# Optimization experiments

Hardware: AMD Instinct MI355X
Metric: run time of the kernel (lower is better)

## Reference

```python
import jax, jax.numpy as jnp
import numpy as np

N_NODES = 50000
N_EDGES = 800000
N_FEAT = 128
HIDDEN = 64
N_CLASSES = 16


def setup_inputs() -> dict:
    key = jax.random.key(0)
    ks = jax.random.split(key, 8)
    x = jax.random.normal(ks[0], (N_NODES, N_FEAT), dtype=jnp.float32)
    edge_index = jax.random.randint(ks[1], (2, N_EDGES), 0, N_NODES, dtype=jnp.int64)
    # GCNConv weights (glorot-like) and biases
    W1 = jax.random.normal(ks[2], (N_FEAT, HIDDEN), dtype=jnp.float32) / np.sqrt(N_FEAT)
    b1 = jnp.zeros((HIDDEN,), dtype=jnp.float32)
    W2 = jax.random.normal(ks[3], (HIDDEN, HIDDEN), dtype=jnp.float32) / np.sqrt(HIDDEN)
    b2 = jnp.zeros((HIDDEN,), dtype=jnp.float32)
    Wout = jax.random.normal(ks[4], (HIDDEN, N_CLASSES), dtype=jnp.float32) / np.sqrt(HIDDEN)
    bout = jnp.zeros((N_CLASSES,), dtype=jnp.float32)
    return {"x": x, "edge_index": edge_index, "W1": W1, "b1": b1,
            "W2": W2, "b2": b2, "Wout": Wout, "bout": bout}


def _gcn_conv(h, src, dst, norm, W, b, n_nodes):
    # h: [N, F_in]; linear transform then normalized scatter-add aggregation
    h = h @ W                                   # [N, F_out]
    msg = h[src] * norm[:, None]                # gather + scale  [E+N, F_out]
    out = jax.ops.segment_sum(msg, dst, num_segments=n_nodes)  # scatter-add
    return out + b


def reference(x, edge_index, W1, b1, W2, b2, Wout, bout):
    n = x.shape[0]
    # add self-loops (PyG GCNConv default add_self_loops=True)
    loops = jnp.arange(n, dtype=edge_index.dtype)
    src = jnp.concatenate([edge_index[0], loops])
    dst = jnp.concatenate([edge_index[1], loops])
    # symmetric normalization: deg^-1/2[src] * deg^-1/2[dst] (edge_weight = 1)
    ones = jnp.ones(src.shape[0], dtype=x.dtype)
    deg = jax.ops.segment_sum(ones, dst, num_segments=n)
    dinv = jnp.where(deg > 0, jax.lax.rsqrt(jnp.maximum(deg, 1e-12)), 0.0)
    norm = dinv[src] * dinv[dst]

    h = _gcn_conv(x, src, dst, norm, W1, b1, n)
    h = jax.nn.relu(h)
    # dropout p=0.5 with training=False -> identity
    h = _gcn_conv(h, src, dst, norm, W2, b2, n)
    h = jax.nn.relu(h)
    logits = h @ Wout + bout
    return jax.nn.softmax(logits, axis=1)
```

## Files before the change

kernel.cpp:

```cpp
#include <hip/hip_runtime.h>
#include <hip/hip_fp16.h>

#define N_NODES 50000
#define N_EDGES 800000
#define N_FEAT 128
#define HIDDEN 64
#define N_CLASSES 16
#define NBLK_NODE 196
#define TCAP 8192

typedef _Float16 f16x8 __attribute__((ext_vector_type(8)));
typedef float f32x4 __attribute__((ext_vector_type(4)));

__global__ void k_init(int* __restrict__ tileCur) {
    int tid = threadIdx.x;
    if (tid < NBLK_NODE) tileCur[tid] = tid * TCAP;
}

__global__ __launch_bounds__(256) void k_part(const int* __restrict__ ei,
                                              int* __restrict__ tileCur,
                                              int* __restrict__ binned) {
    __shared__ int cnt[NBLK_NODE], base[NBLK_NODE], cur[NBLK_NODE];
    int tid = threadIdx.x;
    int start = blockIdx.x * 4096;
    if (tid < NBLK_NODE) cnt[tid] = 0;
    __syncthreads();
    int s[16], d[16];
#pragma unroll
    for (int u = 0; u < 4; ++u) {
        int e0 = start + u * 1024 + tid * 4;
        if (e0 + 4 <= N_EDGES) {
            int4 s4 = *(const int4*)&ei[e0];
            int4 d4 = *(const int4*)&ei[N_EDGES + e0];
            s[u * 4 + 0] = s4.x; s[u * 4 + 1] = s4.y; s[u * 4 + 2] = s4.z; s[u * 4 + 3] = s4.w;
            d[u * 4 + 0] = d4.x; d[u * 4 + 1] = d4.y; d[u * 4 + 2] = d4.z; d[u * 4 + 3] = d4.w;
#pragma unroll
            for (int q = 0; q < 4; ++q) atomicAdd(&cnt[d[u * 4 + q] >> 8], 1);
        } else {
#pragma unroll
            for (int q = 0; q < 4; ++q) {
                int e = e0 + q;
                if (e < N_EDGES) {
                    s[u * 4 + q] = ei[e];
                    d[u * 4 + q] = ei[N_EDGES + e];
                    atomicAdd(&cnt[d[u * 4 + q] >> 8], 1);
                } else s[u * 4 + q] = -1;
            }
        }
    }
    __syncthreads();
    if (tid < NBLK_NODE) {
        base[tid] = atomicAdd(&tileCur[tid], cnt[tid]);
        cur[tid] = 0;
    }
    __syncthreads();
#pragma unroll
    for (int u = 0; u < 16; ++u) {
        if (s[u] < 0) continue;
        int t = d[u] >> 8;
        int r = atomicAdd(&cur[t], 1);
        int p = base[t] + r;
        if (p < (t + 1) * TCAP)
            binned[p] = s[u] | ((d[u] & 255) << 16);
    }
}

__global__ __launch_bounds__(256) void k_finesort(const int* __restrict__ binned,
                                                  const int* __restrict__ tileCur,
                                                  int* __restrict__ csr,
                                                  int2* __restrict__ rse,
                                                  float* __restrict__ dinv) {
    __shared__ int stage[TCAP];
    __shared__ int sc[256];
    __shared__ int cnt256[256];
    __shared__ int nodeOff[256];
    int tid = threadIdx.x;
    int tb = blockIdx.x;
    int beg = tb * TCAP;
    int m = tileCur[tb] - beg;
    if (m > TCAP) m = TCAP;
    cnt256[tid] = 0;
    __syncthreads();
    const int4* b4 = (const int4*)(binned + beg);
    int nv = m >> 2;
    for (int i = tid; i < nv; i += 256) {
        int4 r = b4[i];
        atomicAdd(&cnt256[(r.x >> 16) & 255], 1);
        atomicAdd(&cnt256[(r.y >> 16) & 255], 1);
        atomicAdd(&cnt256[(r.z >> 16) & 255], 1);
        atomicAdd(&cnt256[(r.w >> 16) & 255], 1);
    }
    for (int i = (m & ~3) + tid; i < m; i += 256)
        atomicAdd(&cnt256[(binned[beg + i] >> 16) & 255], 1);
    __syncthreads();
    int myc = cnt256[tid];
    sc[tid] = myc;
    __syncthreads();
#pragma unroll
    for (int off = 1; off < 256; off <<= 1) {
        int t = (tid >= off) ? sc[tid - off] : 0;
        __syncthreads();
        sc[tid] += t;
        __syncthreads();
    }
    int off0 = sc[tid] - myc;
    nodeOff[tid] = off0;
    int gnode = tb * 256 + tid;
    if (gnode < N_NODES) {
        dinv[gnode] = rsqrtf((float)myc + 1.0f);
        rse[gnode] = make_int2(beg + off0, myc);
    }
    cnt256[tid] = 0;
    __syncthreads();
    for (int i = tid; i < nv; i += 256) {
        int4 r = b4[i];
        int rr;
        rr = atomicAdd(&cnt256[(r.x >> 16) & 255], 1); stage[nodeOff[(r.x >> 16) & 255] + rr] = r.x & 0xFFFF;
        rr = atomicAdd(&cnt256[(r.y >> 16) & 255], 1); stage[nodeOff[(r.y >> 16) & 255] + rr] = r.y & 0xFFFF;
        rr = atomicAdd(&cnt256[(r.z >> 16) & 255], 1); stage[nodeOff[(r.z >> 16) & 255] + rr] = r.z & 0xFFFF;
        rr = atomicAdd(&cnt256[(r.w >> 16) & 255], 1); stage[nodeOff[(r.w >> 16) & 255] + rr] = r.w & 0xFFFF;
    }
    for (int i = (m & ~3) + tid; i < m; i += 256) {
        int rec = binned[beg + i];
        int dl = (rec >> 16) & 255;
        int rr = atomicAdd(&cnt256[dl], 1);
        stage[nodeOff[dl] + rr] = rec & 0xFFFF;
    }
    __syncthreads();
    int4* c4 = (int4*)(csr + beg);
    for (int i = tid; i < nv; i += 256) c4[i] = ((const int4*)stage)[i];
    for (int i = (m & ~3) + tid; i < m; i += 256) csr[beg + i] = stage[i];
}

template <int K, typename TIn>
__global__ __launch_bounds__(256) void k_mm(const TIn* __restrict__ a,
                                            const float* __restrict__ w,
                                            const float* __restrict__ dinv,
                                            __half* __restrict__ out) {
    constexpr int LDK = K + 8;
    __shared__ __align__(16) __half A_lds[64 * LDK];
    __shared__ __align__(16) __half Wt_lds[64 * LDK];
    int tid = threadIdx.x;
    long nbase = (long)blockIdx.x * 64;

    for (int i = tid; i < K * 16; i += 256) {
        int k = (i * 4) >> 6;
        int f0 = (i * 4) & 63;
        float4 v = *(const float4*)&w[i * 4];
        Wt_lds[(f0 + 0) * LDK + k] = __float2half(v.x);
        Wt_lds[(f0 + 1) * LDK + k] = __float2half(v.y);
        Wt_lds[(f0 + 2) * LDK + k] = __float2half(v.z);
        Wt_lds[(f0 + 3) * LDK + k] = __float2half(v.w);
    }
    for (int i = tid; i < 64 * K / 8; i += 256) {
        int n = (i * 8) / K;
        int k0 = (i * 8) % K;
        long gn = nbase + n;
        if constexpr (sizeof(TIn) == 4) {
            float4 v0, v1;
            if (gn < N_NODES) {
                v0 = *(const float4*)&a[gn * K + k0];
                v1 = *(const float4*)&a[gn * K + k0 + 4];
            } else {
                v0 = make_float4(0.f, 0.f, 0.f, 0.f);
                v1 = v0;
            }
            __half2* dst = (__half2*)&A_lds[n * LDK + k0];
            dst[0] = __floats2half2_rn(v0.x, v0.y);
            dst[1] = __floats2half2_rn(v0.z, v0.w);
            dst[2] = __floats2half2_rn(v1.x, v1.y);
            dst[3] = __floats2half2_rn(v1.z, v1.w);
        } else {
            int4 v = (gn < N_NODES) ? *(const int4*)&a[gn * K + k0]
                                    : make_int4(0, 0, 0, 0);
            *(int4*)&A_lds[n * LDK + k0] = v;
        }
    }
    __syncthreads();

    int wv = tid >> 6;
    int lane = tid & 63;
    int m = lane & 15;
    int quad = lane >> 4;
    const __half* Arow = &A_lds[(wv * 16 + m) * LDK + quad * 8];
    f32x4 acc[4] = {};
#pragma unroll
    for (int t = 0; t < K; t += 32) {
        f16x8 af = *(const f16x8*)(const void*)&Arow[t];
#pragma unroll
        for (int g = 0; g < 4; ++g) {
            f16x8 bf = *(const f16x8*)(const void*)&Wt_lds[(g * 16 + m) * LDK + t + quad * 8];
            acc[g] = __builtin_amdgcn_mfma_f32_16x16x32_f16(af, bf, acc[g], 0, 0, 0);
        }
    }

#pragma unroll
    for (int r = 0; r < 4; ++r) {
        int n = wv * 16 + quad * 4 + r;
        long gn = nbase + n;
        if (gn < N_NODES) {
            float di = dinv[gn];
#pragma unroll
            for (int g = 0; g < 4; ++g)
                out[gn * HIDDEN + g * 16 + m] = __float2half(acc[g][r] * di);
        }
    }
}

__device__ __forceinline__ void acc_row8(float* a, int4 rv) {
    float2 f;
    f = __half22float2(*(__half2*)&rv.x); a[0] += f.x; a[1] += f.y;
    f = __half22float2(*(__half2*)&rv.y); a[2] += f.x; a[3] += f.y;
    f = __half22float2(*(__half2*)&rv.z); a[4] += f.x; a[5] += f.y;
    f = __half22float2(*(__half2*)&rv.w); a[6] += f.x; a[7] += f.y;
}

__global__ void k_gather(const __half* __restrict__ h, const int* __restrict__ csr,
                         const int2* __restrict__ rse, const float* __restrict__ dinv,
                         const float* __restrict__ bias, __half* __restrict__ out) {
    int t = blockIdx.x * 256 + threadIdx.x;
    int node = __builtin_amdgcn_readfirstlane(t >> 6);
    int lane = t & 63;
    int e8 = lane >> 3;
    int q = lane & 7;
    int2 se = rse[node];
    int r0 = se.x, r1 = se.x + se.y;
    float dd = dinv[node];

    float a[8] = {0.f, 0.f, 0.f, 0.f, 0.f, 0.f, 0.f, 0.f};
    if (e8 == 0)
        acc_row8(a, *(const int4*)&h[(long)node * HIDDEN + q * 8]);

    int j = r0;
    while (j + 16 <= r1) {
        int sA = csr[j + e8];
        int sB = csr[j + 8 + e8];
        int4 rA = *(const int4*)&h[(long)sA * HIDDEN + q * 8];
        int4 rB = *(const int4*)&h[(long)sB * HIDDEN + q * 8];
        acc_row8(a, rA);
        acc_row8(a, rB);
        j += 16;
    }
    if (j + 8 <= r1) {
        int sA = csr[j + e8];
        acc_row8(a, *(const int4*)&h[(long)sA * HIDDEN + q * 8]);
        j += 8;
    }
    int rem = r1 - j;
    if (e8 < rem) {
        int sA = csr[j + e8];
        acc_row8(a, *(const int4*)&h[(long)sA * HIDDEN + q * 8]);
    }
#pragma unroll
    for (int off = 8; off < 64; off <<= 1)
#pragma unroll
        for (int i = 0; i < 8; ++i) a[i] += __shfl_xor(a[i], off, 64);

    if (e8 == 0) {
        float4 b0 = *(const float4*)&bias[q * 8];
        float4 b1 = *(const float4*)&bias[q * 8 + 4];
        float r[8];
        r[0] = fmaxf(fmaf(a[0], dd, b0.x), 0.f);
        r[1] = fmaxf(fmaf(a[1], dd, b0.y), 0.f);
        r[2] = fmaxf(fmaf(a[2], dd, b0.z), 0.f);
        r[3] = fmaxf(fmaf(a[3], dd, b0.w), 0.f);
        r[4] = fmaxf(fmaf(a[4], dd, b1.x), 0.f);
        r[5] = fmaxf(fmaf(a[5], dd, b1.y), 0.f);
        r[6] = fmaxf(fmaf(a[6], dd, b1.z), 0.f);
        r[7] = fmaxf(fmaf(a[7], dd, b1.w), 0.f);
        __half2 h0 = __floats2half2_rn(r[0], r[1]);
        __half2 h1 = __floats2half2_rn(r[2], r[3]);
        __half2 h2 = __floats2half2_rn(r[4], r[5]);
        __half2 h3 = __floats2half2_rn(r[6], r[7]);
        int4 o;
        o.x = *(int*)&h0; o.y = *(int*)&h1; o.z = *(int*)&h2; o.w = *(int*)&h3;
        *(int4*)&out[(long)node * HIDDEN + q * 8] = o;
    }
}

__global__ void k_out(const __half* __restrict__ h, const float* __restrict__ w,
                      const float* __restrict__ b, float* __restrict__ out) {
    __shared__ float Ws[HIDDEN * N_CLASSES];
    __shared__ float bs[N_CLASSES];
    int tid = threadIdx.x;
    for (int i = tid; i < HIDDEN * N_CLASSES; i += 256) Ws[i] = w[i];
    if (tid < N_CLASSES) bs[tid] = b[tid];
    __syncthreads();
    int node = blockIdx.x * 16 + (tid >> 4);
    int c = tid & 15;
    const __half* hr = h + (long)node * HIDDEN;
    float acc = bs[c];
#pragma unroll
    for (int k = 0; k < HIDDEN; ++k)
        acc = fmaf(__half2float(hr[k]), Ws[k * N_CLASSES + c], acc);
    float m = acc;
#pragma unroll
    for (int off = 8; off; off >>= 1) m = fmaxf(m, __shfl_xor(m, off, 16));
    float ex = expf(acc - m);
    float s = ex;
#pragma unroll
    for (int off = 8; off; off >>= 1) s += __shfl_xor(s, off, 16);
    out[(long)node * N_CLASSES + c] = ex / s;
}

extern "C" void kernel_launch(void* const* d_in, const int* in_sizes, int n_in,
                              void* d_out, int out_size, void* d_ws, size_t ws_size,
                              hipStream_t stream) {
    const float* x    = (const float*)d_in[0];
    const int*   ei   = (const int*)d_in[1];
    const float* W1   = (const float*)d_in[2];
    const float* b1   = (const float*)d_in[3];
    const float* W2   = (const float*)d_in[4];
    const float* b2   = (const float*)d_in[5];
    const float* Wout = (const float*)d_in[6];
    const float* bout = (const float*)d_in[7];
    float* out = (float*)d_out;

    char* ws = (char*)d_ws;
    int2*   rse     = (int2*)ws;                       ws += 400128;
    float*  dinv    = (float*)ws;                      ws += 200192;
    int*    tileCur = (int*)ws;                        ws += 1024;
    int*    csr     = (int*)ws;                        ws += (size_t)NBLK_NODE * TCAP * 4;
    char*   slotA   = ws;                              ws += 6553600;
    __half* bufB    = (__half*)ws;
    int*    binned  = (int*)slotA;
    __half* bufA    = (__half*)slotA;

    const int NB_MM = (N_NODES + 63) / 64;
    const int NB_E16 = (N_EDGES + 4095) / 4096;

    k_init<<<1, 256, 0, stream>>>(tileCur);
    k_part<<<NB_E16, 256, 0, stream>>>(ei, tileCur, binned);
    k_finesort<<<NBLK_NODE, 256, 0, stream>>>(binned, tileCur, csr, rse, dinv);

    k_mm<N_FEAT, float><<<NB_MM, 256, 0, stream>>>(x, W1, dinv, bufA);
    k_gather<<<N_NODES / 4, 256, 0, stream>>>(bufA, csr, rse, dinv, b1, bufB);

    k_mm<HIDDEN, __half><<<NB_MM, 256, 0, stream>>>(bufB, W2, dinv, bufA);
    k_gather<<<N_NODES / 4, 256, 0, stream>>>(bufA, csr, rse, dinv, b2, bufB);

    k_out<<<N_NODES / 16, 256, 0, stream>>>(bufB, Wout, bout, out);
}
```

Baseline: 170.5 us.

## Fuse second aggregation with output projection and softmax; single-pass finesort with 512 threads

The second gather kernel now also computes the output linear layer and the softmax in registers. This removes the separate k_out launch and the write and re-read of the hidden fp16 buffer. Separately, the fine sort runs with 512 threads and keeps each record and its atomic rank in registers, so the bin is read from global memory once instead of twice. It also replaces the shared-memory block scan with a wave shuffle scan. The cost is higher register pressure in both kernels, and the fixed 4x512 int4 register loop assumes each tile holds at most TCAP entries.

```diff
diff --git a/kernel.cpp b/kernel.cpp
--- a/kernel.cpp
+++ b/kernel.cpp
@@ -65,71 +65,87 @@
     }
 }
 
-__global__ __launch_bounds__(256) void k_finesort(const int* __restrict__ binned,
+__global__ __launch_bounds__(512) void k_finesort(const int* __restrict__ binned,
                                                   const int* __restrict__ tileCur,
                                                   int* __restrict__ csr,
                                                   int2* __restrict__ rse,
                                                   float* __restrict__ dinv) {
     __shared__ int stage[TCAP];
-    __shared__ int sc[256];
     __shared__ int cnt256[256];
     __shared__ int nodeOff[256];
+    __shared__ int wsum[4];
     int tid = threadIdx.x;
     int tb = blockIdx.x;
     int beg = tb * TCAP;
     int m = tileCur[tb] - beg;
     if (m > TCAP) m = TCAP;
-    cnt256[tid] = 0;
+    if (tid < 256) cnt256[tid] = 0;
     __syncthreads();
     const int4* b4 = (const int4*)(binned + beg);
     int nv = m >> 2;
-    for (int i = tid; i < nv; i += 256) {
-        int4 r = b4[i];
-        atomicAdd(&cnt256[(r.x >> 16) & 255], 1);
-        atomicAdd(&cnt256[(r.y >> 16) & 255], 1);
-        atomicAdd(&cnt256[(r.z >> 16) & 255], 1);
-        atomicAdd(&cnt256[(r.w >> 16) & 255], 1);
-    }
-    for (int i = (m & ~3) + tid; i < m; i += 256)
-        atomicAdd(&cnt256[(binned[beg + i] >> 16) & 255], 1);
-    __syncthreads();
-    int myc = cnt256[tid];
-    sc[tid] = myc;
-    __syncthreads();
-#pragma unroll
-    for (int off = 1; off < 256; off <<= 1) {
-        int t = (tid >= off) ? sc[tid - off] : 0;
-        __syncthreads();
-        sc[tid] += t;
-        __syncthreads();
-    }
-    int off0 = sc[tid] - myc;
-    nodeOff[tid] = off0;
-    int gnode = tb * 256 + tid;
-    if (gnode < N_NODES) {
-        dinv[gnode] = rsqrtf((float)myc + 1.0f);
-        rse[gnode] = make_int2(beg + off0, myc);
-    }
-    cnt256[tid] = 0;
-    __syncthreads();
-    for (int i = tid; i < nv; i += 256) {
-        int4 r = b4[i];
-        int rr;
-        rr = atomicAdd(&cnt256[(r.x >> 16) & 255], 1); stage[nodeOff[(r.x >> 16) & 255] + rr] = r.x & 0xFFFF;
-        rr = atomicAdd(&cnt256[(r.y >> 16) & 255], 1); stage[nodeOff[(r.y >> 16) & 255] + rr] = r.y & 0xFFFF;
-        rr = atomicAdd(&cnt256[(r.z >> 16) & 255], 1); stage[nodeOff[(r.z >> 16) & 255] + rr] = r.z & 0xFFFF;
-        rr = atomicAdd(&cnt256[(r.w >> 16) & 255], 1); stage[nodeOff[(r.w >> 16) & 255] + rr] = r.w & 0xFFFF;
-    }
-    for (int i = (m & ~3) + tid; i < m; i += 256) {
-        int rec = binned[beg + i];
-        int dl = (rec >> 16) & 255;
-        int rr = atomicAdd(&cnt256[dl], 1);
-        stage[nodeOff[dl] + rr] = rec & 0xFFFF;
-    }
+    int4 v[4], rk[4];
+#pragma unroll
+    for (int u = 0; u < 4; ++u) {
+        int i = tid + u * 512;
+        if (i < nv) {
+            int4 r = b4[i];
+            v[u] = r;
+            rk[u].x = atomicAdd(&cnt256[(r.x >> 16) & 255], 1);
+            rk[u].y = atomicAdd(&cnt256[(r.y >> 16) & 255], 1);
+            rk[u].z = atomicAdd(&cnt256[(r.z >> 16) & 255], 1);
+            rk[u].w = atomicAdd(&cnt256[(r.w >> 16) & 255], 1);
+        }
+    }
+    int tailrec = -1, tailrk = 0;
+    int ti = (m & ~3) + tid;
+    if (ti < m) {
+        tailrec = binned[beg + ti];
+        tailrk = atomicAdd(&cnt256[(tailrec >> 16) & 255], 1);
+    }
+    __syncthreads();
+    int myc = 0, sc = 0;
+    if (tid < 256) {
+        myc = cnt256[tid];
+        sc = myc;
+#pragma unroll
+        for (int off = 1; off < 64; off <<= 1) {
+            int tv = __shfl_up(sc, off, 64);
+            if ((tid & 63) >= off) sc += tv;
+        }
+        if ((tid & 63) == 63) wsum[tid >> 6] = sc;
+    }
+    __syncthreads();
+    if (tid < 256) {
+        int wv = tid >> 6;
+        int pre = 0;
+        if (wv > 0) pre += wsum[0];
+        if (wv > 1) pre += wsum[1];
+        if (wv > 2) pre += wsum[2];
+        int off0 = sc - myc + pre;
+        nodeOff[tid] = off0;
+        int gnode = tb * 256 + tid;
+        if (gnode < N_NODES) {
+            dinv[gnode] = rsqrtf((float)myc + 1.0f);
+            rse[gnode] = make_int2(beg + off0, myc);
+        }
+    }
+    __syncthreads();
+#pragma unroll
+    for (int u = 0; u < 4; ++u) {
+        int i = tid + u * 512;
+        if (i < nv) {
+            stage[nodeOff[(v[u].x >> 16) & 255] + rk[u].x] = v[u].x & 0xFFFF;
+            stage[nodeOff[(v[u].y >> 16) & 255] + rk[u].y] = v[u].y & 0xFFFF;
+            stage[nodeOff[(v[u].z >> 16) & 255] + rk[u].z] = v[u].z & 0xFFFF;
+            stage[nodeOff[(v[u].w >> 16) & 255] + rk[u].w] = v[u].w & 0xFFFF;
+        }
+    }
+    if (tailrec >= 0)
+        stage[nodeOff[(tailrec >> 16) & 255] + tailrk] = tailrec & 0xFFFF;
     __syncthreads();
     int4* c4 = (int4*)(csr + beg);
-    for (int i = tid; i < nv; i += 256) c4[i] = ((const int4*)stage)[i];
-    for (int i = (m & ~3) + tid; i < m; i += 256) csr[beg + i] = stage[i];
+    for (int i = tid; i < nv; i += 512) c4[i] = ((const int4*)stage)[i];
+    for (int i = (m & ~3) + tid; i < m; i += 512) csr[beg + i] = stage[i];
 }
 
 template <int K, typename TIn>
@@ -278,29 +294,90 @@
     }
 }
 
-__global__ void k_out(const __half* __restrict__ h, const float* __restrict__ w,
-                      const float* __restrict__ b, float* __restrict__ out) {
-    __shared__ float Ws[HIDDEN * N_CLASSES];
-    __shared__ float bs[N_CLASSES];
-    int tid = threadIdx.x;
-    for (int i = tid; i < HIDDEN * N_CLASSES; i += 256) Ws[i] = w[i];
-    if (tid < N_CLASSES) bs[tid] = b[tid];
-    __syncthreads();
-    int node = blockIdx.x * 16 + (tid >> 4);
-    int c = tid & 15;
-    const __half* hr = h + (long)node * HIDDEN;
-    float acc = bs[c];
-#pragma unroll
-    for (int k = 0; k < HIDDEN; ++k)
-        acc = fmaf(__half2float(hr[k]), Ws[k * N_CLASSES + c], acc);
-    float m = acc;
-#pragma unroll
-    for (int off = 8; off; off >>= 1) m = fmaxf(m, __shfl_xor(m, off, 16));
-    float ex = expf(acc - m);
-    float s = ex;
-#pragma unroll
-    for (int off = 8; off; off >>= 1) s += __shfl_xor(s, off, 16);
-    out[(long)node * N_CLASSES + c] = ex / s;
+__global__ void k_gather_out(const __half* __restrict__ h, const int* __restrict__ csr,
+                             const int2* __restrict__ rse, const float* __restrict__ dinv,
+                             const float* __restrict__ bias,
+                             const float* __restrict__ wout, const float* __restrict__ bout,
+                             float* __restrict__ out) {
+    int t = blockIdx.x * 256 + threadIdx.x;
+    int node = __builtin_amdgcn_readfirstlane(t >> 6);
+    int lane = t & 63;
+    int e8 = lane >> 3;
+    int q = lane & 7;
+    int c0 = e8 * 2;
+    float2 wcol[8];
+#pragma unroll
+    for (int i = 0; i < 8; ++i)
+        wcol[i] = *(const float2*)&wout[(q * 8 + i) * N_CLASSES + c0];
+    float2 bb = *(const float2*)&bout[c0];
+
+    int2 se = rse[node];
+    int r0 = se.x, r1 = se.x + se.y;
+    float dd = dinv[node];
+
+    float a[8] = {0.f, 0.f, 0.f, 0.f, 0.f, 0.f, 0.f, 0.f};
+    if (e8 == 0)
+        acc_row8(a, *(const int4*)&h[(long)node * HIDDEN + q * 8]);
+
+    int j = r0;
+    while (j + 16 <= r1) {
+        int sA = csr[j + e8];
+        int sB = csr[j + 8 + e8];
+        int4 rA = *(const int4*)&h[(long)sA * HIDDEN + q * 8];
+        int4 rB = *(const int4*)&h[(long)sB * HIDDEN + q * 8];
+        acc_row8(a, rA);
+        acc_row8(a, rB);
+        j += 16;
+    }
+    if (j + 8 <= r1) {
+        int sA = csr[j + e8];
+        acc_row8(a, *(const int4*)&h[(long)sA * HIDDEN + q * 8]);
+        j += 8;
+    }
+    int rem = r1 - j;
+    if (e8 < rem) {
+        int sA = csr[j + e8];
+        acc_row8(a, *(const int4*)&h[(long)sA * HIDDEN + q * 8]);
+    }
+#pragma unroll
+    for (int off = 8; off < 64; off <<= 1)
+#pragma unroll
+        for (int i = 0; i < 8; ++i) a[i] += __shfl_xor(a[i], off, 64);
+
+    float4 b0 = *(const float4*)&bias[q * 8];
+    float4 b1 = *(const float4*)&bias[q * 8 + 4];
+    float r[8];
+    r[0] = fmaxf(fmaf(a[0], dd, b0.x), 0.f);
+    r[1] = fmaxf(fmaf(a[1], dd, b0.y), 0.f);
+    r[2] = fmaxf(fmaf(a[2], dd, b0.z), 0.f);
+    r[3] = fmaxf(fmaf(a[3], dd, b0.w), 0.f);
+    r[4] = fmaxf(fmaf(a[4], dd, b1.x), 0.f);
+    r[5] = fmaxf(fmaf(a[5], dd, b1.y), 0.f);
+    r[6] = fmaxf(fmaf(a[6], dd, b1.z), 0.f);
+    r[7] = fmaxf(fmaf(a[7], dd, b1.w), 0.f);
+
+    float l0 = 0.f, l1 = 0.f;
+#pragma unroll
+    for (int i = 0; i < 8; ++i) {
+        l0 = fmaf(r[i], wcol[i].x, l0);
+        l1 = fmaf(r[i], wcol[i].y, l1);
+    }
+#pragma unroll
+    for (int off = 1; off < 8; off <<= 1) {
+        l0 += __shfl_xor(l0, off, 64);
+        l1 += __shfl_xor(l1, off, 64);
+    }
+    l0 += bb.x;
+    l1 += bb.y;
+    float mx = fmaxf(l0, l1);
+#pragma unroll
+    for (int off = 8; off < 64; off <<= 1) mx = fmaxf(mx, __shfl_xor(mx, off, 64));
+    float e0 = expf(l0 - mx), e1 = expf(l1 - mx);
+    float s = e0 + e1;
+#pragma unroll
+    for (int off = 8; off < 64; off <<= 1) s += __shfl_xor(s, off, 64);
+    if (q == 0)
+        *(float2*)&out[(long)node * N_CLASSES + c0] = make_float2(e0 / s, e1 / s);
 }
 
 extern "C" void kernel_launch(void* const* d_in, const int* in_sizes, int n_in,
@@ -331,13 +408,11 @@
 
     k_init<<<1, 256, 0, stream>>>(tileCur);
     k_part<<<NB_E16, 256, 0, stream>>>(ei, tileCur, binned);
-    k_finesort<<<NBLK_NODE, 256, 0, stream>>>(binned, tileCur, csr, rse, dinv);
+    k_finesort<<<NBLK_NODE, 512, 0, stream>>>(binned, tileCur, csr, rse, dinv);
 
     k_mm<N_FEAT, float><<<NB_MM, 256, 0, stream>>>(x, W1, dinv, bufA);
     k_gather<<<N_NODES / 4, 256, 0, stream>>>(bufA, csr, rse, dinv, b1, bufB);
 
     k_mm<HIDDEN, __half><<<NB_MM, 256, 0, stream>>>(bufB, W2, dinv, bufA);
-    k_gather<<<N_NODES / 4, 256, 0, stream>>>(bufA, csr, rse, dinv, b2, bufB);
-
-    k_out<<<N_NODES / 16, 256, 0, stream>>>(bufB, Wout, bout, out);
-}
+    k_gather_out<<<N_NODES / 4, 256, 0, stream>>>(bufA, csr, rse, dinv, b2, Wout, bout, out);
+}
```

Measured after the change: 200.9 us. 17.9% more time.

## Split hidden features into two 32-wide planes for cache-friendly gather

Applied to the files above, without the earlier changes.

Stores the hidden activations as two feature-planes of 32 halves per node instead of one 64-wide row, and splits each gather into two blocks, one per plane. Consecutive blocks (interleaved via blockIdx bits) handle the same plane, so each gather pass touches a working set half the size, meant to improve L2/MALL hit rates for the random neighbour reads. The cost is twice as many gather blocks, each reading the CSR index lists and rse again, and narrower 8-byte loads per lane.

```diff
diff --git a/kernel.cpp b/kernel.cpp
--- a/kernel.cpp
+++ b/kernel.cpp
@@ -8,6 +8,7 @@
 #define N_CLASSES 16
 #define NBLK_NODE 196
 #define TCAP 8192
+#define PLANE (N_NODES * 32)
 
 typedef _Float16 f16x8 __attribute__((ext_vector_type(8)));
 typedef float f32x4 __attribute__((ext_vector_type(4)));
@@ -171,7 +172,8 @@
             dst[2] = __floats2half2_rn(v1.x, v1.y);
             dst[3] = __floats2half2_rn(v1.z, v1.w);
         } else {
-            int4 v = (gn < N_NODES) ? *(const int4*)&a[gn * K + k0]
+            const __half* ap = (const __half*)a + (long)(k0 >> 5) * PLANE;
+            int4 v = (gn < N_NODES) ? *(const int4*)&ap[gn * 32 + (k0 & 31)]
                                     : make_int4(0, 0, 0, 0);
             *(int4*)&A_lds[n * LDK + k0] = v;
         }
@@ -202,79 +204,75 @@
             float di = dinv[gn];
 #pragma unroll
             for (int g = 0; g < 4; ++g)
-                out[gn * HIDDEN + g * 16 + m] = __float2half(acc[g][r] * di);
+                out[(long)(g >> 1) * PLANE + gn * 32 + (g & 1) * 16 + m] =
+                    __float2half(acc[g][r] * di);
         }
     }
 }
 
-__device__ __forceinline__ void acc_row8(float* a, int4 rv) {
+__device__ __forceinline__ void acc_row4(float* a, int2 rv) {
     float2 f;
     f = __half22float2(*(__half2*)&rv.x); a[0] += f.x; a[1] += f.y;
     f = __half22float2(*(__half2*)&rv.y); a[2] += f.x; a[3] += f.y;
-    f = __half22float2(*(__half2*)&rv.z); a[4] += f.x; a[5] += f.y;
-    f = __half22float2(*(__half2*)&rv.w); a[6] += f.x; a[7] += f.y;
 }
 
 __global__ void k_gather(const __half* __restrict__ h, const int* __restrict__ csr,
                          const int2* __restrict__ rse, const float* __restrict__ dinv,
                          const float* __restrict__ bias, __half* __restrict__ out) {
-    int t = blockIdx.x * 256 + threadIdx.x;
-    int node = __builtin_amdgcn_readfirstlane(t >> 6);
+    int b = blockIdx.x;
+    int x = b & 7;
+    int half = x >> 2;
+    int nb = (b >> 3) * 4 + (x & 3);
+    int t = threadIdx.x;
+    int node = __builtin_amdgcn_readfirstlane(nb * 4 + (t >> 6));
     int lane = t & 63;
     int e8 = lane >> 3;
     int q = lane & 7;
+    const __half* hp = h + (long)half * PLANE;
     int2 se = rse[node];
     int r0 = se.x, r1 = se.x + se.y;
     float dd = dinv[node];
 
-    float a[8] = {0.f, 0.f, 0.f, 0.f, 0.f, 0.f, 0.f, 0.f};
+    float a[4] = {0.f, 0.f, 0.f, 0.f};
     if (e8 == 0)
-        acc_row8(a, *(const int4*)&h[(long)node * HIDDEN + q * 8]);
+        acc_row4(a, *(const int2*)&hp[(long)node * 32 + q * 4]);
 
     int j = r0;
     while (j + 16 <= r1) {
         int sA = csr[j + e8];
         int sB = csr[j + 8 + e8];
-        int4 rA = *(const int4*)&h[(long)sA * HIDDEN + q * 8];
-        int4 rB = *(const int4*)&h[(long)sB * HIDDEN + q * 8];
-        acc_row8(a, rA);
-        acc_row8(a, rB);
+        int2 rA = *(const int2*)&hp[(long)sA * 32 + q * 4];
+        int2 rB = *(const int2*)&hp[(long)sB * 32 + q * 4];
+        acc_row4(a, rA);
+        acc_row4(a, rB);
         j += 16;
     }
     if (j + 8 <= r1) {
         int sA = csr[j + e8];
-        acc_row8(a, *(const int4*)&h[(long)sA * HIDDEN + q * 8]);
+        acc_row4(a, *(const int2*)&hp[(long)sA * 32 + q * 4]);
         j += 8;
     }
     int rem = r1 - j;
     if (e8 < rem) {
         int sA = csr[j + e8];
-        acc_row8(a, *(const int4*)&h[(long)sA * HIDDEN + q * 8]);
+        acc_row4(a, *(const int2*)&hp[(long)sA * 32 + q * 4]);
     }
 #pragma unroll
     for (int off = 8; off < 64; off <<= 1)
 #pragma unroll
-        for (int i = 0; i < 8; ++i) a[i] += __shfl_xor(a[i], off, 64);
+        for (int i = 0; i < 4; ++i) a[i] += __shfl_xor(a[i], off, 64);
 
     if (e8 == 0) {
-        float4 b0 = *(const float4*)&bias[q * 8];
-        float4 b1 = *(const float4*)&bias[q * 8 + 4];
-        float r[8];
-        r[0] = fmaxf(fmaf(a[0], dd, b0.x), 0.f);
-        r[1] = fmaxf(fmaf(a[1], dd, b0.y), 0.f);
-        r[2] = fmaxf(fmaf(a[2], dd, b0.z), 0.f);
-        r[3] = fmaxf(fmaf(a[3], dd, b0.w), 0.f);
-        r[4] = fmaxf(fmaf(a[4], dd, b1.x), 0.f);
-        r[5] = fmaxf(fmaf(a[5], dd, b1.y), 0.f);
-        r[6] = fmaxf(fmaf(a[6], dd, b1.z), 0.f);
-        r[7] = fmaxf(fmaf(a[7], dd, b1.w), 0.f);
-        __half2 h0 = __floats2half2_rn(r[0], r[1]);
-        __half2 h1 = __floats2half2_rn(r[2], r[3]);
-        __half2 h2 = __floats2half2_rn(r[4], r[5]);
-        __half2 h3 = __floats2half2_rn(r[6], r[7]);
-        int4 o;
-        o.x = *(int*)&h0; o.y = *(int*)&h1; o.z = *(int*)&h2; o.w = *(int*)&h3;
-        *(int4*)&out[(long)node * HIDDEN + q * 8] = o;
+        float4 bv = *(const float4*)&bias[half * 32 + q * 4];
+        float r0f = fmaxf(fmaf(a[0], dd, bv.x), 0.f);
+        float r1f = fmaxf(fmaf(a[1], dd, bv.y), 0.f);
+        float r2f = fmaxf(fmaf(a[2], dd, bv.z), 0.f);
+        float r3f = fmaxf(fmaf(a[3], dd, bv.w), 0.f);
+        __half2 h0 = __floats2half2_rn(r0f, r1f);
+        __half2 h1 = __floats2half2_rn(r2f, r3f);
+        int2 o;
+        o.x = *(int*)&h0; o.y = *(int*)&h1;
+        *(int2*)&out[(long)half * PLANE + (long)node * 32 + q * 4] = o;
     }
 }
 
@@ -288,11 +286,15 @@
     __syncthreads();
     int node = blockIdx.x * 16 + (tid >> 4);
     int c = tid & 15;
-    const __half* hr = h + (long)node * HIDDEN;
+    const __half* hr0 = h + (long)node * 32;
+    const __half* hr1 = h + (long)PLANE + (long)node * 32;
     float acc = bs[c];
 #pragma unroll
-    for (int k = 0; k < HIDDEN; ++k)
-        acc = fmaf(__half2float(hr[k]), Ws[k * N_CLASSES + c], acc);
+    for (int k = 0; k < 32; ++k)
+        acc = fmaf(__half2float(hr0[k]), Ws[k * N_CLASSES + c], acc);
+#pragma unroll
+    for (int k = 0; k < 32; ++k)
+        acc = fmaf(__half2float(hr1[k]), Ws[(k + 32) * N_CLASSES + c], acc);
     float m = acc;
 #pragma unroll
     for (int off = 8; off; off >>= 1) m = fmaxf(m, __shfl_xor(m, off, 16));
@@ -328,16 +330,17 @@
 
     const int NB_MM = (N_NODES + 63) / 64;
     const int NB_E16 = (N_EDGES + 4095) / 4096;
+    const int NB_GATHER = 2 * (N_NODES / 4);
 
     k_init<<<1, 256, 0, stream>>>(tileCur);
     k_part<<<NB_E16, 256, 0, stream>>>(ei, tileCur, binned);
     k_finesort<<<NBLK_NODE, 256, 0, stream>>>(binned, tileCur, csr, rse, dinv);
 
     k_mm<N_FEAT, float><<<NB_MM, 256, 0, stream>>>(x, W1, dinv, bufA);
-    k_gather<<<N_NODES / 4, 256, 0, stream>>>(bufA, csr, rse, dinv, b1, bufB);
+    k_gather<<<NB_GATHER, 256, 0, stream>>>(bufA, csr, rse, dinv, b1, bufB);
 
     k_mm<HIDDEN, __half><<<NB_MM, 256, 0, stream>>>(bufB, W2, dinv, bufA);
-    k_gather<<<N_NODES / 4, 256, 0, stream>>>(bufA, csr, rse, dinv, b2, bufB);
+    k_gather<<<NB_GATHER, 256, 0, stream>>>(bufA, csr, rse, dinv, b2, bufB);
 
     k_out<<<N_NODES / 16, 256, 0, stream>>>(bufB, Wout, bout, out);
 }
```

Result: slower. 191.4 us (+12.3%).

## Fuse finesort with first matmul and move source dinv scaling into gather

Applied to the files above, without the earlier changes.

Merges the CSR fine-sort kernel and the first feature matmul into one launch with shared dynamic LDS. Blocks below NBLK_NODE sort and the rest compute x@W1, so the two independent stages overlap. To remove the matmul's dependence on dinv, the source-side degree scaling moves into the gather, which now loads dinv[src] per edge and uses FMA. binned now gets its own workspace region instead of aliasing bufA. The cost is an extra scattered dinv load per edge in both gathers.

```diff
diff --git a/kernel.cpp b/kernel.cpp
--- a/kernel.cpp
+++ b/kernel.cpp
@@ -65,17 +65,16 @@
     }
 }
 
-__global__ __launch_bounds__(256) void k_finesort(const int* __restrict__ binned,
-                                                  const int* __restrict__ tileCur,
-                                                  int* __restrict__ csr,
-                                                  int2* __restrict__ rse,
-                                                  float* __restrict__ dinv) {
-    __shared__ int stage[TCAP];
-    __shared__ int sc[256];
-    __shared__ int cnt256[256];
-    __shared__ int nodeOff[256];
-    int tid = threadIdx.x;
-    int tb = blockIdx.x;
+__device__ __forceinline__ void finesort_body(int tb, const int* __restrict__ binned,
+                                              const int* __restrict__ tileCur,
+                                              int* __restrict__ csr,
+                                              int2* __restrict__ rse,
+                                              float* __restrict__ dinv, char* smem) {
+    int* stage   = (int*)smem;
+    int* sc      = stage + TCAP;
+    int* cnt256  = sc + 256;
+    int* nodeOff = cnt256 + 256;
+    int tid = threadIdx.x;
     int beg = tb * TCAP;
     int m = tileCur[tb] - beg;
     if (m > TCAP) m = TCAP;
@@ -133,15 +132,14 @@
 }
 
 template <int K, typename TIn>
-__global__ __launch_bounds__(256) void k_mm(const TIn* __restrict__ a,
-                                            const float* __restrict__ w,
-                                            const float* __restrict__ dinv,
-                                            __half* __restrict__ out) {
+__device__ __forceinline__ void mm_body(int bx, const TIn* __restrict__ a,
+                                        const float* __restrict__ w,
+                                        __half* __restrict__ out, char* smem) {
     constexpr int LDK = K + 8;
-    __shared__ __align__(16) __half A_lds[64 * LDK];
-    __shared__ __align__(16) __half Wt_lds[64 * LDK];
-    int tid = threadIdx.x;
-    long nbase = (long)blockIdx.x * 64;
+    __half* A_lds  = (__half*)smem;
+    __half* Wt_lds = A_lds + 64 * LDK;
+    int tid = threadIdx.x;
+    long nbase = (long)bx * 64;
 
     for (int i = tid; i < K * 16; i += 256) {
         int k = (i * 4) >> 6;
@@ -199,20 +197,42 @@
         int n = wv * 16 + quad * 4 + r;
         long gn = nbase + n;
         if (gn < N_NODES) {
-            float di = dinv[gn];
 #pragma unroll
             for (int g = 0; g < 4; ++g)
-                out[gn * HIDDEN + g * 16 + m] = __float2half(acc[g][r] * di);
+                out[gn * HIDDEN + g * 16 + m] = __float2half(acc[g][r]);
         }
     }
 }
 
-__device__ __forceinline__ void acc_row8(float* a, int4 rv) {
+__global__ __launch_bounds__(256) void k_fsmm1(const int* __restrict__ binned,
+                                               const int* __restrict__ tileCur,
+                                               int* __restrict__ csr,
+                                               int2* __restrict__ rse,
+                                               float* __restrict__ dinv,
+                                               const float* __restrict__ x,
+                                               const float* __restrict__ W1,
+                                               __half* __restrict__ bufA) {
+    __shared__ __align__(16) char smem[35840];
+    int bx = blockIdx.x;
+    if (bx < NBLK_NODE)
+        finesort_body(bx, binned, tileCur, csr, rse, dinv, smem);
+    else
+        mm_body<N_FEAT, float>(bx - NBLK_NODE, x, W1, bufA, smem);
+}
+
+__global__ __launch_bounds__(256) void k_mm2(const __half* __restrict__ a,
+                                             const float* __restrict__ w,
+                                             __half* __restrict__ out) {
+    __shared__ __align__(16) char smem[2 * 64 * (HIDDEN + 8) * 2];
+    mm_body<HIDDEN, __half>(blockIdx.x, a, w, out, smem);
+}
+
+__device__ __forceinline__ void acc_row8s(float* a, int4 rv, float s) {
     float2 f;
-    f = __half22float2(*(__half2*)&rv.x); a[0] += f.x; a[1] += f.y;
-    f = __half22float2(*(__half2*)&rv.y); a[2] += f.x; a[3] += f.y;
-    f = __half22float2(*(__half2*)&rv.z); a[4] += f.x; a[5] += f.y;
-    f = __half22float2(*(__half2*)&rv.w); a[6] += f.x; a[7] += f.y;
+    f = __half22float2(*(__half2*)&rv.x); a[0] = fmaf(f.x, s, a[0]); a[1] = fmaf(f.y, s, a[1]);
+    f = __half22float2(*(__half2*)&rv.y); a[2] = fmaf(f.x, s, a[2]); a[3] = fmaf(f.y, s, a[3]);
+    f = __half22float2(*(__half2*)&rv.z); a[4] = fmaf(f.x, s, a[4]); a[5] = fmaf(f.y, s, a[5]);
+    f = __half22float2(*(__half2*)&rv.w); a[6] = fmaf(f.x, s, a[6]); a[7] = fmaf(f.y, s, a[7]);
 }
 
 __global__ void k_gather(const __half* __restrict__ h, const int* __restrict__ csr,
@@ -229,27 +249,31 @@
 
     float a[8] = {0.f, 0.f, 0.f, 0.f, 0.f, 0.f, 0.f, 0.f};
     if (e8 == 0)
-        acc_row8(a, *(const int4*)&h[(long)node * HIDDEN + q * 8]);
+        acc_row8s(a, *(const int4*)&h[(long)node * HIDDEN + q * 8], dd);
 
     int j = r0;
     while (j + 16 <= r1) {
         int sA = csr[j + e8];
         int sB = csr[j + 8 + e8];
+        float dA = dinv[sA];
+        float dB = dinv[sB];
         int4 rA = *(const int4*)&h[(long)sA * HIDDEN + q * 8];
         int4 rB = *(const int4*)&h[(long)sB * HIDDEN + q * 8];
-        acc_row8(a, rA);
-        acc_row8(a, rB);
+        acc_row8s(a, rA, dA);
+        acc_row8s(a, rB, dB);
         j += 16;
     }
     if (j + 8 <= r1) {
         int sA = csr[j + e8];
-        acc_row8(a, *(const int4*)&h[(long)sA * HIDDEN + q * 8]);
+        float dA = dinv[sA];
+        acc_row8s(a, *(const int4*)&h[(long)sA * HIDDEN + q * 8], dA);
         j += 8;
     }
     int rem = r1 - j;
     if (e8 < rem) {
         int sA = csr[j + e8];
-        acc_row8(a, *(const int4*)&h[(long)sA * HIDDEN + q * 8]);
+        float dA = dinv[sA];
+        acc_row8s(a, *(const int4*)&h[(long)sA * HIDDEN + q * 8], dA);
     }
 #pragma unroll
     for (int off = 8; off < 64; off <<= 1)
@@ -321,22 +345,22 @@
     float*  dinv    = (float*)ws;                      ws += 200192;
     int*    tileCur = (int*)ws;                        ws += 1024;
     int*    csr     = (int*)ws;                        ws += (size_t)NBLK_NODE * TCAP * 4;
-    char*   slotA   = ws;                              ws += 6553600;
+    int*    binned  = (int*)ws;                        ws += (size_t)NBLK_NODE * TCAP * 4;
+    __half* bufA    = (__half*)ws;                     ws += 6553600;
     __half* bufB    = (__half*)ws;
-    int*    binned  = (int*)slotA;
-    __half* bufA    = (__half*)slotA;
 
     const int NB_MM = (N_NODES + 63) / 64;
     const int NB_E16 = (N_EDGES + 4095) / 4096;
 
     k_init<<<1, 256, 0, stream>>>(tileCur);
     k_part<<<NB_E16, 256, 0, stream>>>(ei, tileCur, binned);
-    k_finesort<<<NBLK_NODE, 256, 0, stream>>>(binned, tileCur, csr, rse, dinv);
-
-    k_mm<N_FEAT, float><<<NB_MM, 256, 0, stream>>>(x, W1, dinv, bufA);
+
+    k_fsmm1<<<NBLK_NODE + NB_MM, 256, 0, stream>>>(binned, tileCur, csr, rse, dinv,
+                                                   x, W1, bufA);
+
     k_gather<<<N_NODES / 4, 256, 0, stream>>>(bufA, csr, rse, dinv, b1, bufB);
 
-    k_mm<HIDDEN, __half><<<NB_MM, 256, 0, stream>>>(bufB, W2, dinv, bufA);
+    k_mm2<<<NB_MM, 256, 0, stream>>>(bufB, W2, bufA);
     k_gather<<<N_NODES / 4, 256, 0, stream>>>(bufA, csr, rse, dinv, b2, bufB);
 
     k_out<<<N_NODES / 16, 256, 0, stream>>>(bufB, Wout, bout, out);
```

After: 164.7 us. 3.4% less time.
